# Kernel optimization log

Measured on AMD Instinct MI355X. Metric: run time of the kernel, lower is better.

The kernel has to match this reference:

```python
import jax, jax.numpy as jnp
import numpy as np

N, E, NI, G = 100000, 50000, 2000000, 256
F_IN, H, HOUT, L = 92, 35, 64, 3
NEG = 0.2  # leaky_relu negative_slope (PyG default)


def _seg_softmax(scores, seg, num_seg):
    # PyG softmax grouped by segment id, with +1e-16 in the denominator
    m = jax.ops.segment_max(scores, seg, num_segments=num_seg)
    m = jnp.where(jnp.isfinite(m), m, 0.0)
    ex = jnp.exp(scores - m[seg])
    s = jax.ops.segment_sum(ex, seg, num_segments=num_seg)
    return ex / (s[seg] + 1e-16)


def setup_inputs() -> dict:
    key = jax.random.key(0)
    ks = jax.random.split(key, 10)
    return {
        "x": jax.random.normal(ks[0], (N, F_IN), jnp.float32),
        "hyperedge_attr": jax.random.normal(ks[1], (E, H), jnp.float32),
        "node_idx": jax.random.randint(ks[2], (NI,), 0, N, jnp.int32),
        "edge_idx": jax.random.randint(ks[3], (NI,), 0, E, jnp.int32),
        "batch": jnp.sort(jax.random.randint(ks[4], (N,), 0, G, jnp.int32)),
        "embed_W": jax.random.normal(ks[5], (F_IN, H), jnp.float32) * 0.1,
        "embed_b": jnp.zeros((H,), jnp.float32),
        "lin_W": jax.random.normal(ks[6], (L, H, H), jnp.float32) * 0.17,
        "att": jax.random.normal(ks[7], (L, 2 * H), jnp.float32) * 0.1,
        "conv_b": jnp.zeros((L, H), jnp.float32),
        "proj_W": jax.random.normal(ks[8], (H, HOUT), jnp.float32) * 0.17,
        "proj_b": jnp.zeros((HOUT,), jnp.float32),
        "out_W": jax.random.normal(ks[9], (HOUT, 1), jnp.float32) * 0.12,
        "out_b": jnp.zeros((1,), jnp.float32),
    }


def _hconv(x, he_attr, node_idx, edge_idx, W, att, b):
    # PyG HypergraphConv(use_attention=True, heads=1, attention_mode='node')
    xl = x @ W            # [N, H]  lin (bias=False)
    el = he_attr @ W      # [E, H]  same lin on hyperedge_attr
    s_n = xl @ att[:H]    # [N]  node half of att vector
    s_e = el @ att[H:]    # [E]  edge half of att vector
    alpha = jax.nn.leaky_relu(s_n[node_idx] + s_e[edge_idx], NEG)  # [NI]
    alpha = _seg_softmax(alpha, edge_idx, E)  # softmax over nodes within each hyperedge
    ones = jnp.ones_like(alpha)
    D = jax.ops.segment_sum(ones, node_idx, num_segments=N)   # node degree (hyperedge_weight=1)
    Dinv = jnp.where(D > 0, 1.0 / D, 0.0)
    B = jax.ops.segment_sum(ones, edge_idx, num_segments=E)   # hyperedge size
    Binv = jnp.where(B > 0, 1.0 / B, 0.0)
    # pass 1: node -> hyperedge, message = B_e * alpha * x_v
    m1 = (Binv[edge_idx] * alpha)[:, None] * xl[node_idx]      # [NI, H]
    e_out = jax.ops.segment_sum(m1, edge_idx, num_segments=E)  # [E, H]
    # pass 2: hyperedge -> node, message = D_v * alpha * e_out
    m2 = (Dinv[node_idx] * alpha)[:, None] * e_out[edge_idx]   # [NI, H]
    return jax.ops.segment_sum(m2, node_idx, num_segments=N) + b


def reference(x, hyperedge_attr, node_idx, edge_idx, batch, embed_W, embed_b,
              lin_W, att, conv_b, proj_W, proj_b, out_W, out_b):
    h = x @ embed_W + embed_b                                  # [N, 35]
    for l in range(L):
        h = _hconv(h, hyperedge_attr, node_idx, edge_idx, lin_W[l], att[l], conv_b[l])
    # scatter-mean graph pooling
    s = jax.ops.segment_sum(h, batch, num_segments=G)          # [G, 35]
    cnt = jax.ops.segment_sum(jnp.ones((h.shape[0],), h.dtype), batch, num_segments=G)
    pooled = s / jnp.maximum(cnt, 1.0)[:, None]
    z = jax.nn.softplus(pooled @ proj_W + proj_b)              # [G, 64]
    return z @ out_W + out_b                                   # [G, 1]
```

## Files before the change

### kernel.cpp

```cpp
#include <hip/hip_runtime.h>
#include <hip/hip_bf16.h>
#include <hip/hip_fp16.h>
#include <limits.h>
#include <math.h>

#define F_IN 92
#define H 35
#define HP 36
#define HP2 36
#define HOUT 64
#define NL 3
#define NEG_SLOPE 0.2f
#define NSLICE 8
#define SCH 2048

typedef int iv4 __attribute__((ext_vector_type(4)));


__global__ void embed_kernel(const float* __restrict__ x, const float* __restrict__ W,
                             const float* __restrict__ b, float* __restrict__ h, int N) {
    __shared__ float sW[F_IN * H];
    for (int t = threadIdx.x; t < F_IN * H; t += blockDim.x) sW[t] = W[t];
    __syncthreads();
    int total = N * HP;
    int stride = gridDim.x * blockDim.x;
    for (int t = blockIdx.x * blockDim.x + threadIdx.x; t < total; t += stride) {
        int n = t / HP, j = t - n * HP;
        if (j < H) {
            const float* xr = x + (long)n * F_IN;
            float acc = b[j];
#pragma unroll 4
            for (int k = 0; k < F_IN; ++k) acc += xr[k] * sW[k * H + j];
            h[t] = acc;
        } else {
            h[t] = 0.f;
        }
    }
}

__global__ void lin_h_kernel(const float* __restrict__ in, const float* __restrict__ W,
                             __half* __restrict__ out, int R) {
    __shared__ float sW[H * H];
    for (int t = threadIdx.x; t < H * H; t += blockDim.x) sW[t] = W[t];
    __syncthreads();
    int total = R * HP2;
    int stride = gridDim.x * blockDim.x;
    for (int t = blockIdx.x * blockDim.x + threadIdx.x; t < total; t += stride) {
        int r = t / HP2, j = t - r * HP2;
        if (j < H) {
            const float* ir = in + (long)r * HP;
            float acc = 0.f;
#pragma unroll
            for (int k = 0; k < H; ++k) acc += ir[k] * sW[k * H + j];
            out[t] = __float2half(acc);
        } else {
            out[t] = __float2half(0.f);
        }
    }
}

__global__ void rowdot_kernel(const float* __restrict__ in, const float* __restrict__ vec,
                              float* __restrict__ s, int R, int stride_out) {
    __shared__ float sA[H];
    for (int t = threadIdx.x; t < H; t += blockDim.x) sA[t] = vec[t];
    __syncthreads();
    int stride = gridDim.x * blockDim.x;
    for (int r = blockIdx.x * blockDim.x + threadIdx.x; r < R; r += stride) {
        const float* xr = in + (long)r * HP;
        float acc = 0.f;
#pragma unroll
        for (int k = 0; k < H; ++k) acc += xr[k] * sA[k];
        s[(long)r * stride_out] = acc;
    }
}

__global__ void rowdot_he_kernel(const float* __restrict__ in, const float* __restrict__ vec,
                                 float* __restrict__ s, int R, int stride_out) {
    __shared__ float sA[H];
    for (int t = threadIdx.x; t < H; t += blockDim.x) sA[t] = vec[t];
    __syncthreads();
    int stride = gridDim.x * blockDim.x;
    for (int r = blockIdx.x * blockDim.x + threadIdx.x; r < R; r += stride) {
        const float* xr = in + (long)r * H;
        float acc = 0.f;
#pragma unroll
        for (int k = 0; k < H; ++k) acc += xr[k] * sA[k];
        s[(long)r * stride_out] = acc;
    }
}

__global__ void wfold2_kernel(const float* __restrict__ W, const float* __restrict__ an,
                              const float* __restrict__ ae,
                              float* __restrict__ w1, float* __restrict__ w2) {
    int k = threadIdx.x;
    if (k < H) {
        float acc1 = 0.f, acc2 = 0.f;
#pragma unroll
        for (int j = 0; j < H; ++j) {
            float wkj = W[k * H + j];
            acc1 += wkj * an[j];
            acc2 += wkj * ae[j];
        }
        w1[k] = acc1;
        w2[k] = acc2;
    }
}


__global__ void count_sliced_kernel(const int* __restrict__ ni, const int* __restrict__ ei,
                                    int* __restrict__ ncnt, int* __restrict__ ecnt,
                                    int ninc, int wN, int wE) {
    int s = blockIdx.x & (NSLICE - 1);
    int loN = s * wN, hiN = loN + wN;
    int loE = s * wE, hiE = loE + wE;
    int nblk = gridDim.x >> 3;
    int bid = blockIdx.x >> 3;
    int nvec = ninc >> 2;
    int stride = nblk * blockDim.x;
    for (int q = bid * blockDim.x + threadIdx.x; q < nvec; q += stride) {
        iv4 v4 = __builtin_nontemporal_load((const iv4*)ni + q);
        iv4 e4 = __builtin_nontemporal_load((const iv4*)ei + q);
#pragma unroll
        for (int u = 0; u < 4; ++u) {
            int e = e4[u], v = v4[u];
            if (e >= loE && e < hiE) atomicAdd(&ecnt[e], 1);
            if (v >= loN && v < hiN) atomicAdd(&ncnt[v], 1);
        }
    }
    if (bid == 0) {
        for (int i = (nvec << 2) + threadIdx.x; i < ninc; i += blockDim.x) {
            int v = ni[i], e = ei[i];
            if (e >= loE && e < hiE) atomicAdd(&ecnt[e], 1);
            if (v >= loN && v < hiN) atomicAdd(&ncnt[v], 1);
        }
    }
}

__device__ __forceinline__ int wave_sum_i(int s) {
#pragma unroll
    for (int off = 32; off; off >>= 1) s += __shfl_xor(s, off);
    return s;
}

__global__ void bsum2_kernel(const int* __restrict__ cnt0, int nb0, int n0,
                             const int* __restrict__ cnt1, int n1,
                             int* __restrict__ bsums) {
    int b = blockIdx.x;
    const int* c; int n; int base;
    if (b < nb0) { c = cnt0; n = n0; base = b * SCH; }
    else         { c = cnt1; n = n1; base = (b - nb0) * SCH; }
    int t = threadIdx.x;
    int hi = base + SCH; if (hi > n) hi = n;
    int s = 0;
    for (int i = base + t; i < hi; i += 256) s += c[i];
    s = wave_sum_i(s);
    __shared__ int ws[4];
    if ((t & 63) == 0) ws[t >> 6] = s;
    __syncthreads();
    if (t == 0) bsums[b] = ws[0] + ws[1] + ws[2] + ws[3];
}

__global__ void scan_bsums_kernel(int* __restrict__ bsums, int nb0, int nb1) {
    int t = threadIdx.x;
    if (t == 0) {
        int acc = 0;
        for (int i = 0; i < nb0; ++i) { int v = bsums[i]; bsums[i] = acc; acc += v; }
    } else if (t == 1) {
        int acc = 0;
        for (int i = nb0; i < nb0 + nb1; ++i) { int v = bsums[i]; bsums[i] = acc; acc += v; }
    }
}

__global__ void scan_write2_kernel(const int* __restrict__ cnt0, int* __restrict__ ptr0,
                                   int* __restrict__ cur0, int nb0, int n0,
                                   const int* __restrict__ cnt1, int* __restrict__ ptr1,
                                   int* __restrict__ cur1, int n1,
                                   const int* __restrict__ bsums, int ninc) {
    int b = blockIdx.x;
    const int* c; int* p; int* u; int n; int base;
    if (b < nb0) { c = cnt0; p = ptr0; u = cur0; n = n0; base = b * SCH; }
    else         { c = cnt1; p = ptr1; u = cur1; n = n1; base = (b - nb0) * SCH; }
    int off = bsums[b];
    int t = threadIdx.x;
    int lo = base + t * 8;
    int vals[8];
    int s = 0;
#pragma unroll
    for (int k = 0; k < 8; ++k) {
        int i = lo + k;
        int v = (i < n) ? c[i] : 0;
        vals[k] = s;
        s += v;
    }
    __shared__ int lds[256];
    lds[t] = s;
    __syncthreads();
    for (int o2 = 1; o2 < 256; o2 <<= 1) {
        int v = (t >= o2) ? lds[t - o2] : 0;
        __syncthreads();
        lds[t] += v;
        __syncthreads();
    }
    int tbase = off + ((t == 0) ? 0 : lds[t - 1]);
#pragma unroll
    for (int k = 0; k < 8; ++k) {
        int i = lo + k;
        if (i < n) { int val = tbase + vals[k]; p[i] = val; u[i] = val; }
    }
    if (b == 0 && t == 0) { ptr0[n0] = ninc; ptr1[n1] = ninc; }
}

__global__ void csr_fill_sliced_kernel(const int* __restrict__ ni, const int* __restrict__ ei,
                                       int* __restrict__ ecur, int* __restrict__ ncur,
                                       int* __restrict__ enode, int* __restrict__ nedge,
                                       int ninc, int wN, int wE) {
    int s = blockIdx.x & (NSLICE - 1);
    int loN = s * wN, hiN = loN + wN;
    int loE = s * wE, hiE = loE + wE;
    int nblk = gridDim.x >> 3;
    int bid = blockIdx.x >> 3;
    int nvec = ninc >> 2;
    int stride = nblk * blockDim.x;
    for (int q = bid * blockDim.x + threadIdx.x; q < nvec; q += stride) {
        iv4 v4 = __builtin_nontemporal_load((const iv4*)ni + q);
        iv4 e4 = __builtin_nontemporal_load((const iv4*)ei + q);
#pragma unroll
        for (int u = 0; u < 4; ++u) {
            int e = e4[u], v = v4[u];
            if (e >= loE && e < hiE) {
                int p = atomicAdd(&ecur[e], 1);
                enode[p] = v;
            }
            if (v >= loN && v < hiN) {
                int p = atomicAdd(&ncur[v], 1);
                nedge[p] = e;
            }
        }
    }
    if (bid == 0) {
        for (int i = (nvec << 2) + threadIdx.x; i < ninc; i += blockDim.x) {
            int v = ni[i], e = ei[i];
            if (e >= loE && e < hiE) { int p = atomicAdd(&ecur[e], 1); enode[p] = v; }
            if (v >= loN && v < hiN) { int p = atomicAdd(&ncur[v], 1); nedge[p] = e; }
        }
    }
}


__device__ __forceinline__ float wave_max(float m) {
#pragma unroll
    for (int off = 32; off; off >>= 1) m = fmaxf(m, __shfl_xor(m, off));
    return m;
}
__device__ __forceinline__ float wave_sum(float s) {
#pragma unroll
    for (int off = 32; off; off >>= 1) s += __shfl_xor(s, off);
    return s;
}

__device__ __forceinline__ void grouped_gather_h(const __half* __restrict__ src,
                                                 const float* shA, const int* shV,
                                                 int cnt, int g, int l, float4& acc) {
    if (g < 7) {
        for (int k = g; k < cnt; k += 7) {
            float ak = shA[k];
            int vk = shV[k];
            uint2 raw = ((const uint2*)(src + (size_t)vk * HP2))[l];
            __half2 h01 = *reinterpret_cast<const __half2*>(&raw.x);
            __half2 h23 = *reinterpret_cast<const __half2*>(&raw.y);
            float2 f01 = __half22float2(h01);
            float2 f23 = __half22float2(h23);
            acc.x += ak * f01.x; acc.y += ak * f01.y;
            acc.z += ak * f23.x; acc.w += ak * f23.y;
        }
    }
}

__device__ __forceinline__ void group_reduce(float4& acc, int lane, int l) {
#pragma unroll
    for (int gg = 1; gg < 7; ++gg) {
        int src = l + 9 * gg;
        float ox = __shfl(acc.x, src);
        float oy = __shfl(acc.y, src);
        float oz = __shfl(acc.z, src);
        float ow = __shfl(acc.w, src);
        if (lane < 9) { acc.x += ox; acc.y += oy; acc.z += oz; acc.w += ow; }
    }
}

__global__ void edge_pass_kernel(const int* __restrict__ eptr, const int* __restrict__ enode,
                                 const float* __restrict__ s_n, float* __restrict__ epack,
                                 const __half* __restrict__ xl_h,
                                 __half* __restrict__ e_out_h, int E) {
    __shared__ float shA[4][64];
    __shared__ int   shV[4][64];
    int lane = threadIdx.x & 63;
    int ws = threadIdx.x >> 6;
    int g = lane / 9, l = lane - g * 9;
    int wid = (blockIdx.x * blockDim.x + threadIdx.x) >> 6;
    int nw = (gridDim.x * blockDim.x) >> 6;
    for (int e = wid; e < E; e += nw) {
        int lo = eptr[e], hi = eptr[e + 1];
        int deg = hi - lo;
        float se = epack[4 * (long)e];
        float binv = deg > 0 ? 1.f / (float)deg : 0.f;
        float4 acc = {0.f, 0.f, 0.f, 0.f};
        float mm, rec;
        if (deg <= 64) {
            int v = 0; float sc = -INFINITY;
            if (lane < deg) {
                v = enode[lo + lane];
                sc = s_n[v] + se;
                sc = sc >= 0.f ? sc : NEG_SLOPE * sc;
            }
            float m = wave_max(sc);
            mm = (m == -INFINITY) ? 0.f : m;
            float ex = (lane < deg) ? expf(sc - mm) : 0.f;
            float s = wave_sum(ex);
            rec = 1.f / (s + 1e-16f);
            shA[ws][lane] = ex * rec * binv;
            shV[ws][lane] = v;
            grouped_gather_h(xl_h, shA[ws], shV[ws], deg, g, l, acc);
        } else {
            float m = -INFINITY;
            for (int k = lo + lane; k < hi; k += 64) {
                float sc = s_n[enode[k]] + se;
                sc = sc >= 0.f ? sc : NEG_SLOPE * sc;
                m = fmaxf(m, sc);
            }
            m = wave_max(m);
            mm = (m == -INFINITY) ? 0.f : m;
            float s = 0.f;
            for (int k = lo + lane; k < hi; k += 64) {
                float sc = s_n[enode[k]] + se;
                sc = sc >= 0.f ? sc : NEG_SLOPE * sc;
                s += expf(sc - mm);
            }
            s = wave_sum(s);
            rec = 1.f / (s + 1e-16f);
            float cb = rec * binv;
            for (int base = lo; base < hi; base += 64) {
                int v = 0; float a = 0.f;
                if (base + lane < hi) {
                    v = enode[base + lane];
                    float sc = s_n[v] + se;
                    sc = sc >= 0.f ? sc : NEG_SLOPE * sc;
                    a = expf(sc - mm) * cb;
                }
                shA[ws][lane] = a;
                shV[ws][lane] = v;
                int cn = hi - base; if (cn > 64) cn = 64;
                grouped_gather_h(xl_h, shA[ws], shV[ws], cn, g, l, acc);
            }
        }
        group_reduce(acc, lane, l);
        if (lane < 9) {
            __half2 p0 = __floats2half2_rn(acc.x, acc.y);
            __half2 p1 = __floats2half2_rn(acc.z, acc.w);
            uint2 wv;
            wv.x = *reinterpret_cast<unsigned*>(&p0);
            wv.y = *reinterpret_cast<unsigned*>(&p1);
            ((uint2*)(e_out_h + (size_t)e * HP2))[lane] = wv;
        }
        if (lane == 0) { epack[4 * (long)e + 1] = mm; epack[4 * (long)e + 2] = rec; }
    }
}

__global__ void node_pass_kernel(const int* __restrict__ nptr, const int* __restrict__ nedge,
                                 const float* __restrict__ s_n, const float* __restrict__ epack,
                                 const __half* __restrict__ e_out_h, const float* __restrict__ bias,
                                 float* __restrict__ hout, int N) {
    __shared__ float shA[4][64];
    __shared__ int   shE[4][64];
    __shared__ float sb[HP];
    if (threadIdx.x < HP) sb[threadIdx.x] = (threadIdx.x < H) ? bias[threadIdx.x] : 0.f;
    __syncthreads();
    int lane = threadIdx.x & 63;
    int ws = threadIdx.x >> 6;
    int g = lane / 9, l = lane - g * 9;
    int wid = (blockIdx.x * blockDim.x + threadIdx.x) >> 6;
    int nw = (gridDim.x * blockDim.x) >> 6;
    for (int v = wid; v < N; v += nw) {
        int lo = nptr[v], hi = nptr[v + 1];
        int deg = hi - lo;
        float dinv = deg > 0 ? 1.f / (float)deg : 0.f;
        float sn = s_n[v];
        float4 acc = {0.f, 0.f, 0.f, 0.f};
        if (deg <= 64) {
            int e = 0; float a = 0.f;
            if (lane < deg) {
                e = nedge[lo + lane];
                float4 p = ((const float4*)epack)[e];
                float sc = sn + p.x;
                sc = sc >= 0.f ? sc : NEG_SLOPE * sc;
                a = expf(sc - p.y) * p.z;
            }
            shA[ws][lane] = a;
            shE[ws][lane] = e;
            grouped_gather_h(e_out_h, shA[ws], shE[ws], deg, g, l, acc);
        } else {
            for (int base = lo; base < hi; base += 64) {
                int e = 0; float a = 0.f;
                if (base + lane < hi) {
                    e = nedge[base + lane];
                    float4 p = ((const float4*)epack)[e];
                    float sc = sn + p.x;
                    sc = sc >= 0.f ? sc : NEG_SLOPE * sc;
                    a = expf(sc - p.y) * p.z;
                }
                shA[ws][lane] = a;
                shE[ws][lane] = e;
                int cn = hi - base; if (cn > 64) cn = 64;
                grouped_gather_h(e_out_h, shA[ws], shE[ws], cn, g, l, acc);
            }
        }
        group_reduce(acc, lane, l);
        if (lane < 9) {
            float4 bb = ((const float4*)sb)[lane];
            float4 r;
            r.x = dinv * acc.x + bb.x;
            r.y = dinv * acc.y + bb.y;
            r.z = dinv * acc.z + bb.z;
            r.w = dinv * acc.w + bb.w;
            ((float4*)(hout + (size_t)v * HP))[lane] = r;
        }
    }
}

__global__ void pool_head_kernel(const float* __restrict__ h, const int* __restrict__ batch,
                                 int N, const float* __restrict__ pW, const float* __restrict__ pb,
                                 const float* __restrict__ oW, const float* __restrict__ ob,
                                 float* __restrict__ out) {
    int g = blockIdx.x;
    int t = threadIdx.x;
    __shared__ int bounds[2];
    __shared__ float partial[7][H];
    __shared__ float pooled[H];
    if (t == 0) {
        int lo = 0, hi = N;
        while (lo < hi) { int mid = (lo + hi) >> 1; if (batch[mid] < g) lo = mid + 1; else hi = mid; }
        bounds[0] = lo;
        int lo2 = lo, hi2 = N;
        while (lo2 < hi2) { int mid = (lo2 + hi2) >> 1; if (batch[mid] < g + 1) lo2 = mid + 1; else hi2 = mid; }
        bounds[1] = lo2;
    }
    __syncthreads();
    int rlo = bounds[0], rhi = bounds[1];
    int cntg = rhi - rlo;
    int gg = t / H;
    int j = t - gg * H;
    if (gg < 7) {
        float acc = 0.f;
        for (int r = rlo + gg; r < rhi; r += 7) acc += h[(long)r * HP + j];
        partial[gg][j] = acc;
    }
    __syncthreads();
    if (t < H) {
        float s = 0.f;
#pragma unroll
        for (int k = 0; k < 7; ++k) s += partial[k][t];
        pooled[t] = s / fmaxf((float)cntg, 1.f);
    }
    __syncthreads();
    if (t < HOUT) {
        float acc = pb[t];
#pragma unroll
        for (int k = 0; k < H; ++k) acc += pooled[k] * pW[k * HOUT + t];
        float z = fmaxf(acc, 0.f) + log1pf(expf(-fabsf(acc)));
        float pr = z * oW[t];
#pragma unroll
        for (int off = 32; off; off >>= 1) pr += __shfl_down(pr, off);
        if (t == 0) out[g] = pr + ob[0];
    }
}

static inline int grid_for(long n, int block = 256, long cap = 2048) {
    long b = (n + block - 1) / block;
    if (b > cap) b = cap;
    if (b < 1) b = 1;
    return (int)b;
}

extern "C" void kernel_launch(void* const* d_in, const int* in_sizes, int n_in,
                              void* d_out, int out_size, void* d_ws, size_t ws_size,
                              hipStream_t stream) {
    const float* x       = (const float*)d_in[0];
    const float* he      = (const float*)d_in[1];
    const int*   ni      = (const int*)d_in[2];
    const int*   ei      = (const int*)d_in[3];
    const int*   batch   = (const int*)d_in[4];
    const float* embed_W = (const float*)d_in[5];
    const float* embed_b = (const float*)d_in[6];
    const float* lin_W   = (const float*)d_in[7];
    const float* att     = (const float*)d_in[8];
    const float* conv_b  = (const float*)d_in[9];
    const float* proj_W  = (const float*)d_in[10];
    const float* proj_b  = (const float*)d_in[11];
    const float* out_W   = (const float*)d_in[12];
    const float* out_b   = (const float*)d_in[13];
    float* out = (float*)d_out;

    const int N    = in_sizes[0] / F_IN;
    const int E    = in_sizes[1] / H;
    const int NINC = in_sizes[2];
    const int G    = out_size;

    char* w = (char*)d_ws;
    auto alloc = [&](size_t bytes) {
        char* p = w;
        w += (bytes + 255) & ~(size_t)255;
        return p;
    };
    float*  h       = (float*)alloc((size_t)N * HP * 4);
    __half* xl_h    = (__half*)alloc((size_t)N * HP2 * 2);
    __half* e_out_h = (__half*)alloc((size_t)E * HP2 * 2);
    float*  s_n     = (float*)alloc((size_t)N * 4);
    float*  epack   = (float*)alloc((size_t)E * 16);
    float*  w1      = (float*)alloc((size_t)H * 4);
    float*  w2      = (float*)alloc((size_t)H * 4);
    int*    ecnt    = (int*)alloc((size_t)E * 4);
    int*    eptr    = (int*)alloc((size_t)(E + 1) * 4);
    int*    ecur    = (int*)alloc((size_t)E * 4);
    int*    ncnt    = (int*)alloc((size_t)N * 4);
    int*    nptr    = (int*)alloc((size_t)(N + 1) * 4);
    int*    ncur    = (int*)alloc((size_t)N * 4);
    int*    enode   = (int*)alloc((size_t)NINC * 4);
    int*    nedge   = (int*)alloc((size_t)NINC * 4);
    int*    bsums   = (int*)alloc((size_t)256 * 4);

    const int BLK = 256;
    int gNH  = grid_for((long)N * HP);
    int gN   = grid_for(N);
    int gE   = grid_for(E);
    int wN   = (N + NSLICE - 1) / NSLICE;
    int wE   = (E + NSLICE - 1) / NSLICE;
    int nbE  = (E + SCH - 1) / SCH;
    int nbN  = (N + SCH - 1) / SCH;

    (void)hipMemsetAsync(ncnt, 0, (size_t)N * 4, stream);
    (void)hipMemsetAsync(ecnt, 0, (size_t)E * 4, stream);
    count_sliced_kernel<<<2048, BLK, 0, stream>>>(ni, ei, ncnt, ecnt, NINC, wN, wE);
    bsum2_kernel<<<nbE + nbN, 256, 0, stream>>>(ecnt, nbE, E, ncnt, N, bsums);
    scan_bsums_kernel<<<1, 64, 0, stream>>>(bsums, nbE, nbN);
    scan_write2_kernel<<<nbE + nbN, 256, 0, stream>>>(ecnt, eptr, ecur, nbE, E,
                                                      ncnt, nptr, ncur, N, bsums, NINC);
    csr_fill_sliced_kernel<<<2048, BLK, 0, stream>>>(ni, ei, ecur, ncur, enode, nedge,
                                                     NINC, wN, wE);

    embed_kernel<<<gNH, BLK, 0, stream>>>(x, embed_W, embed_b, h, N);

    int gEdge = (E + 3) / 4;
    int gNode = (N + 3) / 4;
    for (int l = 0; l < NL; ++l) {
        const float* W  = lin_W + (size_t)l * H * H;
        const float* at = att + (size_t)l * 2 * H;
        const float* b  = conv_b + (size_t)l * H;

        lin_h_kernel<<<gNH, BLK, 0, stream>>>(h, W, xl_h, N);
        wfold2_kernel<<<1, 64, 0, stream>>>(W, at, at + H, w1, w2);
        rowdot_kernel<<<gN, BLK, 0, stream>>>(h, w1, s_n, N, 1);
        rowdot_he_kernel<<<gE, BLK, 0, stream>>>(he, w2, epack, E, 4);

        edge_pass_kernel<<<gEdge, BLK, 0, stream>>>(eptr, enode, s_n, epack, xl_h, e_out_h, E);
        node_pass_kernel<<<gNode, BLK, 0, stream>>>(nptr, nedge, s_n, epack, e_out_h, b, h, N);
    }

    pool_head_kernel<<<G, BLK, 0, stream>>>(h, batch, N, proj_W, proj_b, out_W, out_b, out);
}
```

Baseline: 940.3 us.

## Fuse next-layer linear and node score into node pass and embed epilogues

Removes the separate per-layer lin_h and rowdot kernels. After a node's aggregated row is finished in node_pass (or in the embedding), the same wavefront multiplies it by the next layer's weight to produce the fp16 xl row and the node attention score. All weight/att folds are precomputed once in a single kernel. This avoids re-reading h from global memory twice per layer and cuts launches. In exchange node_pass carries more shared memory and per-row compute, and relies on wave-synchronous LDS exchange with no barrier.

```diff
diff --git a/kernel.cpp b/kernel.cpp
--- a/kernel.cpp
+++ b/kernel.cpp
@@ -16,61 +16,24 @@
 
 typedef int iv4 __attribute__((ext_vector_type(4)));
 
-
-__global__ void embed_kernel(const float* __restrict__ x, const float* __restrict__ W,
-                             const float* __restrict__ b, float* __restrict__ h, int N) {
-    __shared__ float sW[F_IN * H];
-    for (int t = threadIdx.x; t < F_IN * H; t += blockDim.x) sW[t] = W[t];
-    __syncthreads();
-    int total = N * HP;
-    int stride = gridDim.x * blockDim.x;
-    for (int t = blockIdx.x * blockDim.x + threadIdx.x; t < total; t += stride) {
-        int n = t / HP, j = t - n * HP;
-        if (j < H) {
-            const float* xr = x + (long)n * F_IN;
-            float acc = b[j];
-#pragma unroll 4
-            for (int k = 0; k < F_IN; ++k) acc += xr[k] * sW[k * H + j];
-            h[t] = acc;
-        } else {
-            h[t] = 0.f;
-        }
-    }
-}
-
-__global__ void lin_h_kernel(const float* __restrict__ in, const float* __restrict__ W,
-                             __half* __restrict__ out, int R) {
-    __shared__ float sW[H * H];
-    for (int t = threadIdx.x; t < H * H; t += blockDim.x) sW[t] = W[t];
-    __syncthreads();
-    int total = R * HP2;
-    int stride = gridDim.x * blockDim.x;
-    for (int t = blockIdx.x * blockDim.x + threadIdx.x; t < total; t += stride) {
-        int r = t / HP2, j = t - r * HP2;
-        if (j < H) {
-            const float* ir = in + (long)r * HP;
-            float acc = 0.f;
-#pragma unroll
-            for (int k = 0; k < H; ++k) acc += ir[k] * sW[k * H + j];
-            out[t] = __float2half(acc);
-        } else {
-            out[t] = __float2half(0.f);
-        }
-    }
-}
-
-__global__ void rowdot_kernel(const float* __restrict__ in, const float* __restrict__ vec,
-                              float* __restrict__ s, int R, int stride_out) {
-    __shared__ float sA[H];
-    for (int t = threadIdx.x; t < H; t += blockDim.x) sA[t] = vec[t];
-    __syncthreads();
-    int stride = gridDim.x * blockDim.x;
-    for (int r = blockIdx.x * blockDim.x + threadIdx.x; r < R; r += stride) {
-        const float* xr = in + (long)r * HP;
-        float acc = 0.f;
-#pragma unroll
-        for (int k = 0; k < H; ++k) acc += xr[k] * sA[k];
-        s[(long)r * stride_out] = acc;
+__global__ void wfold_all_kernel(const float* __restrict__ lin_W, const float* __restrict__ att,
+                                 float* __restrict__ w1, float* __restrict__ w2) {
+    int k = threadIdx.x;
+    if (k < H) {
+        for (int l = 0; l < NL; ++l) {
+            const float* W  = lin_W + (size_t)l * H * H;
+            const float* an = att + (size_t)l * 2 * H;
+            const float* ae = an + H;
+            float a1 = 0.f, a2 = 0.f;
+#pragma unroll
+            for (int j = 0; j < H; ++j) {
+                float wkj = W[k * H + j];
+                a1 += wkj * an[j];
+                a2 += wkj * ae[j];
+            }
+            w1[l * H + k] = a1;
+            w2[l * H + k] = a2;
+        }
     }
 }
 
@@ -89,20 +52,48 @@
     }
 }
 
-__global__ void wfold2_kernel(const float* __restrict__ W, const float* __restrict__ an,
-                              const float* __restrict__ ae,
-                              float* __restrict__ w1, float* __restrict__ w2) {
-    int k = threadIdx.x;
-    if (k < H) {
-        float acc1 = 0.f, acc2 = 0.f;
-#pragma unroll
-        for (int j = 0; j < H; ++j) {
-            float wkj = W[k * H + j];
-            acc1 += wkj * an[j];
-            acc2 += wkj * ae[j];
-        }
-        w1[k] = acc1;
-        w2[k] = acc2;
+__global__ void embed_fused_kernel(const float* __restrict__ x, const float* __restrict__ eW,
+                                   const float* __restrict__ eb, const float* __restrict__ W0,
+                                   const float* __restrict__ w1_0,
+                                   float* __restrict__ h, __half* __restrict__ xl_h,
+                                   float* __restrict__ s_n, int N) {
+    __shared__ float sEW[F_IN * H];
+    __shared__ float sW[H * H];
+    __shared__ float sw1[H];
+    __shared__ float sb[H];
+    __shared__ float shrow[4][HP];
+    __shared__ __half shh[4][HP];
+    for (int t = threadIdx.x; t < F_IN * H; t += blockDim.x) sEW[t] = eW[t];
+    for (int t = threadIdx.x; t < H * H; t += blockDim.x) sW[t] = W0[t];
+    if (threadIdx.x < H) { sw1[threadIdx.x] = w1_0[threadIdx.x]; sb[threadIdx.x] = eb[threadIdx.x]; }
+    __syncthreads();
+    int lane = threadIdx.x & 63, ws = threadIdx.x >> 6;
+    int wid = (blockIdx.x * blockDim.x + threadIdx.x) >> 6;
+    int nw = (gridDim.x * blockDim.x) >> 6;
+    for (int n = wid; n < N; n += nw) {
+        const float* xr = x + (long)n * F_IN;
+        if (lane < H) {
+            float acc = sb[lane];
+#pragma unroll 4
+            for (int k = 0; k < F_IN; ++k) acc += xr[k] * sEW[k * H + lane];
+            shrow[ws][lane] = acc;
+        } else if (lane == H) {
+            shrow[ws][H] = 0.f;
+        }
+        if (lane < 9) ((float4*)(h + (size_t)n * HP))[lane] = ((const float4*)&shrow[ws][0])[lane];
+        if (lane < H) {
+            float a = 0.f;
+#pragma unroll
+            for (int k = 0; k < H; ++k) a += shrow[ws][k] * sW[k * H + lane];
+            shh[ws][lane] = __float2half(a);
+        } else if (lane == H) {
+            float a2 = 0.f;
+#pragma unroll
+            for (int k = 0; k < H; ++k) a2 += shrow[ws][k] * sw1[k];
+            s_n[n] = a2;
+            shh[ws][H] = __float2half(0.f);
+        }
+        if (lane < 9) ((uint2*)(xl_h + (size_t)n * HP2))[lane] = ((const uint2*)&shh[ws][0])[lane];
     }
 }
 
@@ -367,13 +358,22 @@
 }
 
 __global__ void node_pass_kernel(const int* __restrict__ nptr, const int* __restrict__ nedge,
-                                 const float* __restrict__ s_n, const float* __restrict__ epack,
+                                 const float* __restrict__ s_n_in, const float* __restrict__ epack,
                                  const __half* __restrict__ e_out_h, const float* __restrict__ bias,
-                                 float* __restrict__ hout, int N) {
+                                 const float* __restrict__ Wn, const float* __restrict__ w1n,
+                                 int produce,
+                                 float* __restrict__ hout, __half* __restrict__ xl_out,
+                                 float* __restrict__ snout, int N) {
     __shared__ float shA[4][64];
     __shared__ int   shE[4][64];
     __shared__ float sb[HP];
+    __shared__ float sW[H * H];
+    __shared__ float sw1[H];
+    __shared__ float shrow[4][HP];
+    __shared__ __half shh[4][HP];
     if (threadIdx.x < HP) sb[threadIdx.x] = (threadIdx.x < H) ? bias[threadIdx.x] : 0.f;
+    for (int t = threadIdx.x; t < H * H; t += blockDim.x) sW[t] = Wn[t];
+    if (threadIdx.x < H) sw1[threadIdx.x] = w1n[threadIdx.x];
     __syncthreads();
     int lane = threadIdx.x & 63;
     int ws = threadIdx.x >> 6;
@@ -384,7 +384,7 @@
         int lo = nptr[v], hi = nptr[v + 1];
         int deg = hi - lo;
         float dinv = deg > 0 ? 1.f / (float)deg : 0.f;
-        float sn = s_n[v];
+        float sn = s_n_in[v];
         float4 acc = {0.f, 0.f, 0.f, 0.f};
         if (deg <= 64) {
             int e = 0; float a = 0.f;
@@ -423,6 +423,22 @@
             r.z = dinv * acc.z + bb.z;
             r.w = dinv * acc.w + bb.w;
             ((float4*)(hout + (size_t)v * HP))[lane] = r;
+            ((float4*)&shrow[ws][0])[lane] = r;
+        }
+        if (produce) {
+            if (lane < H) {
+                float a = 0.f;
+#pragma unroll
+                for (int k = 0; k < H; ++k) a += shrow[ws][k] * sW[k * H + lane];
+                shh[ws][lane] = __float2half(a);
+            } else if (lane == H) {
+                float a2 = 0.f;
+#pragma unroll
+                for (int k = 0; k < H; ++k) a2 += shrow[ws][k] * sw1[k];
+                snout[v] = a2;
+                shh[ws][H] = __float2half(0.f);
+            }
+            if (lane < 9) ((uint2*)(xl_out + (size_t)v * HP2))[lane] = ((const uint2*)&shh[ws][0])[lane];
         }
     }
 }
@@ -516,8 +532,8 @@
     __half* e_out_h = (__half*)alloc((size_t)E * HP2 * 2);
     float*  s_n     = (float*)alloc((size_t)N * 4);
     float*  epack   = (float*)alloc((size_t)E * 16);
-    float*  w1      = (float*)alloc((size_t)H * 4);
-    float*  w2      = (float*)alloc((size_t)H * 4);
+    float*  w1      = (float*)alloc((size_t)NL * H * 4);
+    float*  w2      = (float*)alloc((size_t)NL * H * 4);
     int*    ecnt    = (int*)alloc((size_t)E * 4);
     int*    eptr    = (int*)alloc((size_t)(E + 1) * 4);
     int*    ecur    = (int*)alloc((size_t)E * 4);
@@ -529,8 +545,6 @@
     int*    bsums   = (int*)alloc((size_t)256 * 4);
 
     const int BLK = 256;
-    int gNH  = grid_for((long)N * HP);
-    int gN   = grid_for(N);
     int gE   = grid_for(E);
     int wN   = (N + NSLICE - 1) / NSLICE;
     int wE   = (E + NSLICE - 1) / NSLICE;
@@ -547,22 +561,24 @@
     csr_fill_sliced_kernel<<<2048, BLK, 0, stream>>>(ni, ei, ecur, ncur, enode, nedge,
                                                      NINC, wN, wE);
 
-    embed_kernel<<<gNH, BLK, 0, stream>>>(x, embed_W, embed_b, h, N);
+    wfold_all_kernel<<<1, 64, 0, stream>>>(lin_W, att, w1, w2);
+    int gRow = (N + 3) / 4;
+    embed_fused_kernel<<<gRow, BLK, 0, stream>>>(x, embed_W, embed_b, lin_W, w1,
+                                                 h, xl_h, s_n, N);
 
     int gEdge = (E + 3) / 4;
     int gNode = (N + 3) / 4;
     for (int l = 0; l < NL; ++l) {
-        const float* W  = lin_W + (size_t)l * H * H;
-        const float* at = att + (size_t)l * 2 * H;
-        const float* b  = conv_b + (size_t)l * H;
-
-        lin_h_kernel<<<gNH, BLK, 0, stream>>>(h, W, xl_h, N);
-        wfold2_kernel<<<1, 64, 0, stream>>>(W, at, at + H, w1, w2);
-        rowdot_kernel<<<gN, BLK, 0, stream>>>(h, w1, s_n, N, 1);
-        rowdot_he_kernel<<<gE, BLK, 0, stream>>>(he, w2, epack, E, 4);
-
+        const float* b = conv_b + (size_t)l * H;
+        int lnext = (l + 1 < NL) ? l + 1 : l;
+        const float* Wn  = lin_W + (size_t)lnext * H * H;
+        const float* w1n = w1 + (size_t)lnext * H;
+        int produce = (l + 1 < NL) ? 1 : 0;
+
+        rowdot_he_kernel<<<gE, BLK, 0, stream>>>(he, w2 + (size_t)l * H, epack, E, 4);
         edge_pass_kernel<<<gEdge, BLK, 0, stream>>>(eptr, enode, s_n, epack, xl_h, e_out_h, E);
-        node_pass_kernel<<<gNode, BLK, 0, stream>>>(nptr, nedge, s_n, epack, e_out_h, b, h, N);
+        node_pass_kernel<<<gNode, BLK, 0, stream>>>(nptr, nedge, s_n, epack, e_out_h, b,
+                                                    Wn, w1n, produce, h, xl_h, s_n, N);
     }
 
     pool_head_kernel<<<G, BLK, 0, stream>>>(h, batch, N, proj_W, proj_b, out_W, out_b, out);
```

New measurement: 1.159 ms. 1.23x slower.

## Fuse next-layer linear transform and node scores into node pass epilogue

Applied to the files above, without the earlier changes.

The node pass epilogue now computes the next layer's xl (h·W, stored as half) and the node attention score from the freshly written row. This removes the separate lin_h and rowdot launches, and their re-read of h, for layers 2 and 3. The per-layer weight folding is also precomputed for all layers in a single launch. In exchange, every node-pass block stages the 35x35 weight matrix into shared memory, which is a lot of redundant traffic across many small blocks, and the epilogue does a serial 35-term dot product per lane.

```diff
diff --git a/kernel.cpp b/kernel.cpp
--- a/kernel.cpp
+++ b/kernel.cpp
@@ -89,20 +89,24 @@
     }
 }
 
-__global__ void wfold2_kernel(const float* __restrict__ W, const float* __restrict__ an,
-                              const float* __restrict__ ae,
-                              float* __restrict__ w1, float* __restrict__ w2) {
+__global__ void wfold_all_kernel(const float* __restrict__ lin_W, const float* __restrict__ att,
+                                 float* __restrict__ w1, float* __restrict__ w2) {
     int k = threadIdx.x;
     if (k < H) {
-        float acc1 = 0.f, acc2 = 0.f;
-#pragma unroll
-        for (int j = 0; j < H; ++j) {
-            float wkj = W[k * H + j];
-            acc1 += wkj * an[j];
-            acc2 += wkj * ae[j];
-        }
-        w1[k] = acc1;
-        w2[k] = acc2;
+        for (int l = 0; l < NL; ++l) {
+            const float* W  = lin_W + (size_t)l * H * H;
+            const float* an = att + (size_t)l * 2 * H;
+            const float* ae = an + H;
+            float a1 = 0.f, a2 = 0.f;
+#pragma unroll
+            for (int j = 0; j < H; ++j) {
+                float wkj = W[k * H + j];
+                a1 += wkj * an[j];
+                a2 += wkj * ae[j];
+            }
+            w1[l * H + k] = a1;
+            w2[l * H + k] = a2;
+        }
     }
 }
 
@@ -367,13 +371,24 @@
 }
 
 __global__ void node_pass_kernel(const int* __restrict__ nptr, const int* __restrict__ nedge,
-                                 const float* __restrict__ s_n, const float* __restrict__ epack,
+                                 const float* __restrict__ s_n_in, const float* __restrict__ epack,
                                  const __half* __restrict__ e_out_h, const float* __restrict__ bias,
-                                 float* __restrict__ hout, int N) {
+                                 const float* __restrict__ Wn, const float* __restrict__ w1n,
+                                 int produce,
+                                 float* __restrict__ hout, __half* __restrict__ xl_out,
+                                 float* __restrict__ snout, int N) {
     __shared__ float shA[4][64];
     __shared__ int   shE[4][64];
     __shared__ float sb[HP];
+    __shared__ float sW[H * H];
+    __shared__ float sw1[H];
+    __shared__ float shrow[4][HP];
+    __shared__ __half shh[4][HP];
     if (threadIdx.x < HP) sb[threadIdx.x] = (threadIdx.x < H) ? bias[threadIdx.x] : 0.f;
+    if (produce) {
+        for (int t = threadIdx.x; t < H * H; t += blockDim.x) sW[t] = Wn[t];
+        if (threadIdx.x < H) sw1[threadIdx.x] = w1n[threadIdx.x];
+    }
     __syncthreads();
     int lane = threadIdx.x & 63;
     int ws = threadIdx.x >> 6;
@@ -384,7 +399,7 @@
         int lo = nptr[v], hi = nptr[v + 1];
         int deg = hi - lo;
         float dinv = deg > 0 ? 1.f / (float)deg : 0.f;
-        float sn = s_n[v];
+        float sn = s_n_in[v];
         float4 acc = {0.f, 0.f, 0.f, 0.f};
         if (deg <= 64) {
             int e = 0; float a = 0.f;
@@ -423,6 +438,22 @@
             r.z = dinv * acc.z + bb.z;
             r.w = dinv * acc.w + bb.w;
             ((float4*)(hout + (size_t)v * HP))[lane] = r;
+            if (produce) ((float4*)&shrow[ws][0])[lane] = r;
+        }
+        if (produce) {
+            if (lane < H) {
+                float a = 0.f;
+#pragma unroll
+                for (int k = 0; k < H; ++k) a += shrow[ws][k] * sW[k * H + lane];
+                shh[ws][lane] = __float2half(a);
+            } else if (lane == H) {
+                float a2 = 0.f;
+#pragma unroll
+                for (int k = 0; k < H; ++k) a2 += shrow[ws][k] * sw1[k];
+                snout[v] = a2;
+                shh[ws][H] = __float2half(0.f);
+            }
+            if (lane < 9) ((uint2*)(xl_out + (size_t)v * HP2))[lane] = ((const uint2*)&shh[ws][0])[lane];
         }
     }
 }
@@ -516,8 +547,8 @@
     __half* e_out_h = (__half*)alloc((size_t)E * HP2 * 2);
     float*  s_n     = (float*)alloc((size_t)N * 4);
     float*  epack   = (float*)alloc((size_t)E * 16);
-    float*  w1      = (float*)alloc((size_t)H * 4);
-    float*  w2      = (float*)alloc((size_t)H * 4);
+    float*  w1      = (float*)alloc((size_t)NL * H * 4);
+    float*  w2      = (float*)alloc((size_t)NL * H * 4);
     int*    ecnt    = (int*)alloc((size_t)E * 4);
     int*    eptr    = (int*)alloc((size_t)(E + 1) * 4);
     int*    ecur    = (int*)alloc((size_t)E * 4);
@@ -547,22 +578,24 @@
     csr_fill_sliced_kernel<<<2048, BLK, 0, stream>>>(ni, ei, ecur, ncur, enode, nedge,
                                                      NINC, wN, wE);
 
+    wfold_all_kernel<<<1, 64, 0, stream>>>(lin_W, att, w1, w2);
     embed_kernel<<<gNH, BLK, 0, stream>>>(x, embed_W, embed_b, h, N);
+    lin_h_kernel<<<gNH, BLK, 0, stream>>>(h, lin_W, xl_h, N);
+    rowdot_kernel<<<gN, BLK, 0, stream>>>(h, w1, s_n, N, 1);
 
     int gEdge = (E + 3) / 4;
     int gNode = (N + 3) / 4;
     for (int l = 0; l < NL; ++l) {
-        const float* W  = lin_W + (size_t)l * H * H;
-        const float* at = att + (size_t)l * 2 * H;
-        const float* b  = conv_b + (size_t)l * H;
-
-        lin_h_kernel<<<gNH, BLK, 0, stream>>>(h, W, xl_h, N);
-        wfold2_kernel<<<1, 64, 0, stream>>>(W, at, at + H, w1, w2);
-        rowdot_kernel<<<gN, BLK, 0, stream>>>(h, w1, s_n, N, 1);
-        rowdot_he_kernel<<<gE, BLK, 0, stream>>>(he, w2, epack, E, 4);
-
+        const float* b = conv_b + (size_t)l * H;
+        int lnext = (l + 1 < NL) ? l + 1 : l;
+        const float* Wn  = lin_W + (size_t)lnext * H * H;
+        const float* w1n = w1 + (size_t)lnext * H;
+        int produce = (l + 1 < NL) ? 1 : 0;
+
+        rowdot_he_kernel<<<gE, BLK, 0, stream>>>(he, w2 + (size_t)l * H, epack, E, 4);
         edge_pass_kernel<<<gEdge, BLK, 0, stream>>>(eptr, enode, s_n, epack, xl_h, e_out_h, E);
-        node_pass_kernel<<<gNode, BLK, 0, stream>>>(nptr, nedge, s_n, epack, e_out_h, b, h, N);
+        node_pass_kernel<<<gNode, BLK, 0, stream>>>(nptr, nedge, s_n, epack, e_out_h, b,
+                                                    Wn, w1n, produce, h, xl_h, s_n, N);
     }
 
     pool_head_kernel<<<G, BLK, 0, stream>>>(h, batch, N, proj_W, proj_b, out_W, out_b, out);
```

New measurement: 1.066 ms. 1.13x slower.
